# Kernel optimization log

Hardware: AMD Instinct MI355X
Metric: run time of the kernel (lower is better)

Reference implementation:

```python
import jax, jax.numpy as jnp
import numpy as np
import math

B, S, D, H = 8, 512, 1024, 16
HD = D // H  # 64
FF = 4 * D
EPS = 1e-5


def setup_inputs() -> dict:
    key = jax.random.key(0)
    ks = jax.random.split(key, 12)
    sc = 0.02
    return {
        "x":   jax.random.normal(ks[0], (B, S, D), jnp.float32),
        "Wq":  jax.random.normal(ks[1], (H, D, HD), jnp.float32) * sc,
        "Wk":  jax.random.normal(ks[2], (H, D, HD), jnp.float32) * sc,
        "Wv":  jax.random.normal(ks[3], (H, D, HD), jnp.float32) * sc,
        "Wo":  jax.random.normal(ks[4], (D, D), jnp.float32) * sc,
        "bo":  jnp.zeros((D,), jnp.float32),
        "g1":  jnp.ones((D,), jnp.float32),
        "b1":  jnp.zeros((D,), jnp.float32),
        "g2":  jnp.ones((D,), jnp.float32),
        "b2":  jnp.zeros((D,), jnp.float32),
        "W1":  jax.random.normal(ks[5], (D, FF), jnp.float32) * sc,
        "bf1": jnp.zeros((FF,), jnp.float32),
        "W2":  jax.random.normal(ks[6], (FF, D), jnp.float32) * sc,
        "bf2": jnp.zeros((D,), jnp.float32),
    }


def _layernorm(x, gamma, beta):
    # biased variance, matches torch.var(correction=0)
    mean = jnp.mean(x, axis=-1, keepdims=True)
    var = jnp.mean((x - mean) ** 2, axis=-1, keepdims=True)
    return (x - mean) / jnp.sqrt(var + EPS) * gamma + beta


def _block(x, Wq, Wk, Wv, Wo, bo, g1, b1, g2, b2, W1, bf1, W2, bf2):
    h = _layernorm(x, g1, b1)
    # per-head projections (no bias): [B,H,S,HD]
    Q = jnp.einsum("bsd,hde->bhse", h, Wq)
    K = jnp.einsum("bsd,hde->bhse", h, Wk)
    V = jnp.einsum("bsd,hde->bhse", h, Wv)
    scores = jnp.einsum("bhse,bhte->bhst", Q, K) / math.sqrt(HD)
    causal = jnp.triu(jnp.ones((S, S), bool), k=1)  # upper-triangular masked
    scores = jnp.where(causal, jnp.float32(-1e10), scores)
    att = jax.nn.softmax(scores, axis=-1)  # dropout in eval mode = identity
    ctx = jnp.einsum("bhst,bhte->bhse", att, V)
    # concat heads in order -> [B,S,D]
    ctx = ctx.transpose(0, 2, 1, 3).reshape(B, S, D)
    attn_out = ctx @ Wo + bo
    cache = attn_out + x
    h2 = _layernorm(cache, g2, b2)
    ff = jax.nn.gelu(h2 @ W1 + bf1, approximate=False) @ W2 + bf2
    return ff + cache


def reference(x, Wq, Wk, Wv, Wo, bo, g1, b1, g2, b2, W1, bf1, W2, bf2):
    return _block(x, Wq, Wk, Wv, Wo, bo, g1, b1, g2, b2, W1, bf1, W2, bf2)
```

## Files before the change

### kernel.cpp

```cpp
#include <hip/hip_runtime.h>
#include <hip/hip_bf16.h>

typedef __hip_bfloat16 bf16;

#define B_   8
#define S_   512
#define D_   1024
#define H_   16
#define HD_  64
#define FF_  4096
#define ROWS (B_ * S_)

typedef __attribute__((ext_vector_type(8))) unsigned short u16x8;
typedef __attribute__((ext_vector_type(4))) float f32x4;

typedef __attribute__((address_space(1))) const unsigned int GU32;
typedef __attribute__((address_space(3))) unsigned int LU32;
__device__ __forceinline__ void gld16(const void* g, void* l) {
    __builtin_amdgcn_global_load_lds((GU32*)g, (LU32*)l, 16, 0, 0);
}

__device__ __forceinline__ float bf2f(unsigned short u) {
    union { unsigned int i; float f; } v; v.i = ((unsigned int)u) << 16; return v.f;
}
__device__ __forceinline__ unsigned short f2bfu(float f) {
    bf16 h = __float2bfloat16(f);
    return *reinterpret_cast<unsigned short*>(&h);
}
__device__ __forceinline__ float ldsel(const void* p, size_t i, bool f32) {
    return f32 ? ((const float*)p)[i]
               : __bfloat162float(((const bf16*)p)[i]);
}
__device__ __forceinline__ float gelu_exact(float x) {
    return 0.5f * x * (1.f + erff(x * 0.70710678118654752440f));
}

__global__ __launch_bounds__(256) void ln_kernel(const void* __restrict__ x,
                                                 const void* __restrict__ gam,
                                                 const void* __restrict__ bet,
                                                 bf16* __restrict__ out,
                                                 int x_ws,
                                                 const unsigned short* __restrict__ probe) {
    bool pf32 = (probe[0] == 0);
    bool xf32 = (!x_ws) && pf32;
    int row = blockIdx.x;
    int tid = threadIdx.x;
    size_t rb = (size_t)row * D_;
    float v[4];
#pragma unroll
    for (int i = 0; i < 4; ++i) v[i] = ldsel(x, rb + tid + i * 256, xf32);
    float s  = v[0] + v[1] + v[2] + v[3];
    float s2 = v[0] * v[0] + v[1] * v[1] + v[2] * v[2] + v[3] * v[3];
#pragma unroll
    for (int off = 32; off > 0; off >>= 1) {
        s  += __shfl_down(s, off);
        s2 += __shfl_down(s2, off);
    }
    __shared__ float red[8];
    int wv = tid >> 6, ln = tid & 63;
    if (ln == 0) { red[wv] = s; red[4 + wv] = s2; }
    __syncthreads();
    s  = red[0] + red[1] + red[2] + red[3];
    s2 = red[4] + red[5] + red[6] + red[7];
    float mean = s * (1.f / 1024.f);
    float var  = s2 * (1.f / 1024.f) - mean * mean;
    float rstd = rsqrtf(var + 1e-5f);
#pragma unroll
    for (int i = 0; i < 4; ++i) {
        int c = tid + i * 256;
        float g = ldsel(gam, c, pf32), b = ldsel(bet, c, pf32);
        out[rb + c] = __float2bfloat16((v[i] - mean) * rstd * g + b);
    }
}

__global__ __launch_bounds__(256) void transpose_kernel(
    const void* __restrict__ src, bf16* __restrict__ dst,
    int N, int K, int sK, int sH,
    const unsigned short* __restrict__ probe) {
    bool pf32 = (probe[0] == 0);
    int tilesN = N >> 6;
    int tn = blockIdx.x % tilesN, tk = blockIdx.x / tilesN;
    int n0 = tn * 64, k0 = tk * 64;
    __shared__ float T[64][65];
    int t = threadIdx.x;
    size_t headoff = (size_t)(n0 >> 6) * sH;
#pragma unroll
    for (int i = 0; i < 16; ++i) {
        int lin = t + i * 256;
        int kl = lin >> 6, nl = lin & 63;
        size_t e = headoff + (size_t)(k0 + kl) * sK + nl;
        T[kl][nl] = ldsel(src, e, pf32);
    }
    __syncthreads();
#pragma unroll
    for (int i = 0; i < 16; ++i) {
        int lin = t + i * 256;
        int nl = lin >> 6, kl = lin & 63;
        dst[(size_t)(n0 + nl) * K + k0 + kl] = __float2bfloat16(T[kl][nl]);
    }
}

template<int BN>
__global__ __launch_bounds__(256) void gemm_mfma(
    const bf16* __restrict__ A, const bf16* __restrict__ Bt,
    int K, int nSeg, int segShift, size_t segStride,
    const void* __restrict__ bias,
    const void* __restrict__ resid, int resid_ws,
    bf16* __restrict__ outWS, void* __restrict__ outFinal, int mode,
    const unsigned short* __restrict__ probe) {
    constexpr int BM     = 128;
    constexpr int NR     = BN / 32;
    constexpr int PLANES = (BN == 64) ? 2 : 1;
    constexpr int KSTEP  = 32 * PLANES;
    constexpr int CPP    = 8 + BN / 16;
    constexpr int NCH    = PLANES * CPP / 4;
    constexpr int APL    = BM * 32;
    constexpr int BPL    = BN * 32;
    constexpr int AREG   = 2 * PLANES * APL;
    bool pf32 = (probe[0] == 0);
    __shared__ alignas(16) unsigned short SMEM[2 * PLANES * (BM + BN) * 32];
    int tid  = threadIdx.x;
    int lane = tid & 63, wv = tid >> 6;
    int g = lane >> 4, i16 = lane & 15;
    int wrow = wv >> 1, wcol = wv & 1;

    int GX = gridDim.x;
    int total = GX * gridDim.y;
    int bid = blockIdx.y * GX + blockIdx.x;
    int swz = bid;
    if ((total & 7) == 0) swz = (bid & 7) * (total >> 3) + (bid >> 3);
    int m0 = (swz / GX) * BM, n0 = (swz % GX) * BN;

    f32x4 acc[4][NR];
#pragma unroll
    for (int i = 0; i < 4; ++i)
#pragma unroll
        for (int j = 0; j < NR; ++j) acc[i][j] = (f32x4){0.f, 0.f, 0.f, 0.f};

    const unsigned short* gsrc[NCH];
    unsigned short* l0[NCH];
    unsigned short* l1[NCH];
    {
        int rl = lane >> 2, kq = (lane & 3) * 8;
#pragma unroll
        for (int c0 = 0; c0 < NCH; ++c0) {
            int c = c0 * 4 + wv;
            int pl = c / CPP, cc = c - pl * CPP;
            if (cc < 8) {
                gsrc[c0] = (const unsigned short*)A
                         + (size_t)(m0 + cc * 16 + rl) * K + pl * 32 + kq;
                l0[c0] = &SMEM[(0 * PLANES + pl) * APL + cc * 512];
                l1[c0] = &SMEM[(1 * PLANES + pl) * APL + cc * 512];
            } else {
                gsrc[c0] = (const unsigned short*)Bt
                         + (size_t)(n0 + (cc - 8) * 16 + rl) * K + pl * 32 + kq;
                l0[c0] = &SMEM[AREG + (0 * PLANES + pl) * BPL + (cc - 8) * 512];
                l1[c0] = &SMEM[AREG + (1 * PLANES + pl) * BPL + (cc - 8) * 512];
            }
        }
    }

#define STAGE0(KOFF) { _Pragma("unroll") \
    for (int c0 = 0; c0 < NCH; ++c0) gld16(gsrc[c0] + (KOFF), l0[c0]); }
#define STAGE1(KOFF) { _Pragma("unroll") \
    for (int c0 = 0; c0 < NCH; ++c0) gld16(gsrc[c0] + (KOFF), l1[c0]); }
#define COMPUTE(BUF) { \
    _Pragma("unroll") \
    for (int pl = 0; pl < PLANES; ++pl) { \
        u16x8 af[4], bfv[NR]; \
        _Pragma("unroll") \
        for (int i = 0; i < 4; ++i) \
            af[i] = *reinterpret_cast<const u16x8*>( \
                &SMEM[((BUF) * PLANES + pl) * APL + (wrow * 64 + i * 16 + i16) * 32 + g * 8]); \
        _Pragma("unroll") \
        for (int j = 0; j < NR; ++j) \
            bfv[j] = *reinterpret_cast<const u16x8*>( \
                &SMEM[AREG + ((BUF) * PLANES + pl) * BPL + (wcol * (BN / 2) + j * 16 + i16) * 32 + g * 8]); \
        _Pragma("unroll") \
        for (int i = 0; i < 4; ++i) \
            _Pragma("unroll") \
            for (int j = 0; j < NR; ++j) \
                asm("v_mfma_f32_16x16x32_bf16 %0, %1, %2, %0" \
                    : "+v"(acc[i][j]) : "v"(af[i]), "v"(bfv[j])); \
    } }

    STAGE0(0);
    __syncthreads();
    for (int k0 = 0; k0 < K; k0 += 2 * KSTEP) {
        STAGE1(k0 + KSTEP);
        COMPUTE(0);
        __syncthreads();
        if (k0 + 2 * KSTEP < K) STAGE0(k0 + 2 * KSTEP);
        COMPUTE(1);
        __syncthreads();
    }
#undef STAGE0
#undef STAGE1
#undef COMPUTE

    __builtin_amdgcn_sched_barrier(0);
    asm volatile("s_nop 7\n\ts_nop 7\n\ts_nop 7" ::: );
    __builtin_amdgcn_sched_barrier(0);

    if (outFinal && pf32) {
        int coll = i16, rowl = g * 4;
#pragma unroll
        for (int j = 0; j < NR; ++j) {
            int n = n0 + wcol * (BN / 2) + j * 16 + coll;
            int nl = n & (nSeg - 1);
            float bval = (mode != 0) ? ldsel(bias, nl, pf32) : 0.f;
#pragma unroll
            for (int i = 0; i < 4; ++i) {
                int mb = m0 + wrow * 64 + i * 16 + rowl;
#pragma unroll
                for (int r = 0; r < 4; ++r) {
                    size_t idx = (size_t)(mb + r) * nSeg + nl;
                    float c = acc[i][j][r];
                    if (mode == 1) {
                        c += bval;
                        c += resid_ws ? __bfloat162float(((const bf16*)resid)[idx])
                                      : ldsel(resid, idx, pf32);
                    } else if (mode == 2) {
                        c = gelu_exact(c + bval);
                    }
                    ((float*)outFinal)[idx] = c;
                }
            }
        }
    } else {
        unsigned short* Cs = SMEM;
        int seg = n0 >> segShift;
        int nl0 = n0 & (nSeg - 1);
        bf16* dst = outFinal ? (bf16*)outFinal
                             : outWS + (size_t)seg * segStride;
#pragma unroll
        for (int j = 0; j < NR; ++j) {
            int nloc = wcol * (BN / 2) + j * 16 + i16;
            int nl = nl0 + nloc;
            float bval = (mode != 0) ? ldsel(bias, nl, pf32) : 0.f;
#pragma unroll
            for (int i = 0; i < 4; ++i) {
#pragma unroll
                for (int r = 0; r < 4; ++r) {
                    int mloc = wrow * 64 + i * 16 + g * 4 + r;
                    float c = acc[i][j][r];
                    if (mode == 1) {
                        size_t idx = (size_t)(m0 + mloc) * nSeg + nl;
                        c += bval;
                        c += resid_ws ? __bfloat162float(((const bf16*)resid)[idx])
                                      : ldsel(resid, idx, pf32);
                    } else if (mode == 2) {
                        c = gelu_exact(c + bval);
                    }
                    int swzC = ((((mloc >> 2) & 3) ^ (mloc & 3)) << 4);
                    Cs[mloc * BN + (nloc ^ swzC)] = f2bfu(c);
                }
            }
        }
        __syncthreads();
        constexpr int NP = (BM * BN) / 2048;
#pragma unroll
        for (int p = 0; p < NP; ++p) {
            int lin = p * 2048 + tid * 8;
            int m = lin / BN, nn = lin % BN;
            int swzC = ((((m >> 2) & 3) ^ (m & 3)) << 4);
            u16x8 v = *reinterpret_cast<const u16x8*>(&Cs[m * BN + (nn ^ swzC)]);
            *reinterpret_cast<u16x8*>(dst + (size_t)(m0 + m) * nSeg + nl0 + nn) = v;
        }
    }
}

__global__ __launch_bounds__(256) void attn_kernel(const bf16* __restrict__ Qg,
                                                   const bf16* __restrict__ Kg,
                                                   const bf16* __restrict__ Vg,
                                                   bf16* __restrict__ Og) {
    constexpr int P = 72;
    __shared__ alignas(16) unsigned short Ks[64 * P];
    __shared__ alignas(16) unsigned short Vt[64 * P];
    __shared__ alignas(16) unsigned short Ps[64 * P];
    int qb = blockIdx.x;
    int bh = blockIdx.y;
    int b = bh >> 4, h = bh & 15;
    int tid = threadIdx.x;
    int lane = tid & 63, wv = tid >> 6;
    int g = lane >> 4, i16 = lane & 15;
    size_t base = ((size_t)b * S_) * D_ + h * HD_;

    u16x8 qa[2];
    {
        const unsigned short* qp = (const unsigned short*)Qg + base
            + (size_t)(qb * 64 + wv * 16 + i16) * D_ + g * 8;
#pragma unroll
        for (int kk = 0; kk < 2; ++kk) {
            u16x8 v = *reinterpret_cast<const u16x8*>(qp + kk * 32);
#pragma unroll
            for (int e = 0; e < 8; ++e) v[e] = f2bfu(bf2f(v[e]) * 0.125f);
            qa[kk] = v;
        }
    }
    f32x4 ov[4];
#pragma unroll
    for (int dj = 0; dj < 4; ++dj) ov[dj] = (f32x4){0.f, 0.f, 0.f, 0.f};
    float mrow[4], lrow[4];
#pragma unroll
    for (int r = 0; r < 4; ++r) { mrow[r] = -1e30f; lrow[r] = 0.f; }

    int st = tid >> 2, sd = (tid & 3) * 16;
    const unsigned short* Kp = (const unsigned short*)Kg + base + (size_t)st * D_ + sd;
    const unsigned short* Vp = (const unsigned short*)Vg + base + (size_t)st * D_ + sd;
    unsigned short* KsW = &Ks[st * P + sd];
    unsigned short* VtW = &Vt[sd * P + (st ^ sd)];
    int g1 = g >> 1, g0 = g & 1;
    unsigned short* PsW = &Ps[(wv * 16 + g * 4) * P + (i16 ^ (g0 << 3))];
    const unsigned short* PsR = &Ps[(wv * 16 + i16) * P + ((g ^ ((i16 >> 2) & 3)) << 3)];

    for (int kb = 0; kb <= qb; ++kb) {
        __syncthreads();
        size_t ko = (size_t)kb * 64 * D_;
        u16x8 k0 = *reinterpret_cast<const u16x8*>(Kp + ko);
        u16x8 k1 = *reinterpret_cast<const u16x8*>(Kp + ko + 8);
        u16x8 v0 = *reinterpret_cast<const u16x8*>(Vp + ko);
        u16x8 v1 = *reinterpret_cast<const u16x8*>(Vp + ko + 8);
        *reinterpret_cast<u16x8*>(KsW)     = k0;
        *reinterpret_cast<u16x8*>(KsW + 8) = k1;
#pragma unroll
        for (int ii = 0; ii < 8; ++ii) VtW[ii * P] = v0[ii];
#pragma unroll
        for (int ii = 0; ii < 8; ++ii) VtW[(ii + 8) * P] = v1[ii];
        __syncthreads();

        f32x4 sc[4];
#pragma unroll
        for (int tj = 0; tj < 4; ++tj) sc[tj] = (f32x4){0.f, 0.f, 0.f, 0.f};
#pragma unroll
        for (int kk = 0; kk < 2; ++kk)
#pragma unroll
            for (int tj = 0; tj < 4; ++tj) {
                u16x8 kf = *reinterpret_cast<const u16x8*>(
                    &Ks[(tj * 16 + i16) * P + kk * 32 + g * 8]);
                asm("v_mfma_f32_16x16x32_bf16 %0, %1, %2, %0"
                    : "+v"(sc[tj]) : "v"(qa[kk]), "v"(kf));
            }
        __builtin_amdgcn_sched_barrier(0);
        asm volatile("s_nop 7\n\ts_nop 7\n\ts_nop 7" ::: );
        __builtin_amdgcn_sched_barrier(0);

        if (kb == qb) {
#pragma unroll
            for (int tj = 0; tj < 4; ++tj)
#pragma unroll
                for (int r = 0; r < 4; ++r)
                    if (tj * 16 + i16 > wv * 16 + g * 4 + r) sc[tj][r] = -1e30f;
        }
        float al[4];
#pragma unroll
        for (int r = 0; r < 4; ++r) {
            float mt = fmaxf(fmaxf(sc[0][r], sc[1][r]), fmaxf(sc[2][r], sc[3][r]));
            mt = fmaxf(mt, __shfl_xor(mt, 1));
            mt = fmaxf(mt, __shfl_xor(mt, 2));
            mt = fmaxf(mt, __shfl_xor(mt, 4));
            mt = fmaxf(mt, __shfl_xor(mt, 8));
            float mnew = fmaxf(mrow[r], mt);
            al[r] = __expf(mrow[r] - mnew);
            mrow[r] = mnew;
        }
        float psum[4] = {0.f, 0.f, 0.f, 0.f};
        unsigned short pw[4][4];
#pragma unroll
        for (int tj = 0; tj < 4; ++tj)
#pragma unroll
            for (int r = 0; r < 4; ++r) {
                float p = __expf(sc[tj][r] - mrow[r]);
                unsigned short pb = f2bfu(p);
                pw[tj][r] = pb;
                psum[r] += bf2f(pb);
            }
#pragma unroll
        for (int r = 0; r < 4; ++r) {
            float ps = psum[r];
            ps += __shfl_xor(ps, 1);
            ps += __shfl_xor(ps, 2);
            ps += __shfl_xor(ps, 4);
            ps += __shfl_xor(ps, 8);
            lrow[r] = lrow[r] * al[r] + ps;
        }
#pragma unroll
        for (int dj = 0; dj < 4; ++dj)
#pragma unroll
            for (int r = 0; r < 4; ++r) ov[dj][r] *= al[r];
#pragma unroll
        for (int r = 0; r < 4; ++r)
#pragma unroll
            for (int tj = 0; tj < 4; ++tj)
                PsW[r * P + ((tj ^ g1) << 4)] = pw[tj][r];
#pragma unroll
        for (int kk = 0; kk < 2; ++kk) {
            u16x8 pf = *reinterpret_cast<const u16x8*>(PsR + kk * 32);
#pragma unroll
            for (int dj = 0; dj < 4; ++dj) {
                int tcol = ((kk << 5) | (g << 3)) ^ (dj << 4);
                u16x8 vf = *reinterpret_cast<const u16x8*>(
                    &Vt[(dj * 16 + i16) * P + tcol]);
                asm("v_mfma_f32_16x16x32_bf16 %0, %1, %2, %0"
                    : "+v"(ov[dj]) : "v"(pf), "v"(vf));
            }
        }
    }
    __builtin_amdgcn_sched_barrier(0);
    asm volatile("s_nop 7\n\ts_nop 7\n\ts_nop 7" ::: );
    __builtin_amdgcn_sched_barrier(0);
    float rl[4];
#pragma unroll
    for (int r = 0; r < 4; ++r) rl[r] = 1.f / lrow[r];
    bf16* op = Og + base + (size_t)(qb * 64 + wv * 16 + g * 4) * D_ + i16;
#pragma unroll
    for (int r = 0; r < 4; ++r)
#pragma unroll
        for (int dj = 0; dj < 4; ++dj)
            op[(size_t)r * D_ + dj * 16] = __float2bfloat16(ov[dj][r] * rl[r]);
}

extern "C" void kernel_launch(void* const* d_in, const int* in_sizes, int n_in,
                              void* d_out, int out_size, void* d_ws, size_t ws_size,
                              hipStream_t stream) {
    const void* x   = d_in[0];
    const void* Wq  = d_in[1];
    const void* Wk  = d_in[2];
    const void* Wv  = d_in[3];
    const void* Wo  = d_in[4];
    const void* bo  = d_in[5];
    const void* g1  = d_in[6];
    const void* b1  = d_in[7];
    const void* g2  = d_in[8];
    const void* b2  = d_in[9];
    const void* W1  = d_in[10];
    const void* bf1 = d_in[11];
    const void* W2  = d_in[12];
    const void* bf2 = d_in[13];
    const unsigned short* probe = (const unsigned short*)g1;

    bf16* ws = (bf16*)d_ws;
    const size_t Mi = (size_t)1024 * 1024;
    bf16* h     = ws;
    bf16* Qb    = ws + 4 * Mi;
    bf16* Kb    = ws + 8 * Mi;
    bf16* Vb    = ws + 12 * Mi;
    bf16* ctx   = ws;
    bf16* cache = ws + 4 * Mi;
    bf16* h2    = ws + 8 * Mi;
    bf16* ff1   = ws + 12 * Mi;
    bf16* WqT   = ws + 16 * Mi;
    bf16* WkT   = ws + 17 * Mi;
    bf16* WvT   = ws + 18 * Mi;
    bf16* WoT   = ws + 19 * Mi;
    bf16* W1T   = ws;
    bf16* W2T   = ws + 8 * Mi;

    transpose_kernel<<<256, 256, 0, stream>>>(Wq, WqT, 1024, 1024, HD_, D_ * HD_, probe);
    transpose_kernel<<<256, 256, 0, stream>>>(Wk, WkT, 1024, 1024, HD_, D_ * HD_, probe);
    transpose_kernel<<<256, 256, 0, stream>>>(Wv, WvT, 1024, 1024, HD_, D_ * HD_, probe);
    transpose_kernel<<<256, 256, 0, stream>>>(Wo, WoT, 1024, 1024, 1024, 64, probe);
    ln_kernel<<<ROWS, 256, 0, stream>>>(x, g1, b1, h, 0, probe);
    gemm_mfma<128><<<dim3(3072 / 128, ROWS / 128), 256, 0, stream>>>(
        h, WqT, 1024, 1024, 10, 4 * Mi,
        nullptr, nullptr, 0, Qb, nullptr, 0, probe);
    dim3 gA(S_ / 64, B_ * H_);
    attn_kernel<<<gA, 256, 0, stream>>>(Qb, Kb, Vb, ctx);
    gemm_mfma<64><<<dim3(1024 / 64, ROWS / 128), 256, 0, stream>>>(
        ctx, WoT, 1024, 1024, 30, 0,
        bo, x, 0, cache, nullptr, 1, probe);
    transpose_kernel<<<1024, 256, 0, stream>>>(W1, W1T, 4096, 1024, FF_, 64, probe);
    ln_kernel<<<ROWS, 256, 0, stream>>>(cache, g2, b2, h2, 1, probe);
    gemm_mfma<128><<<dim3(4096 / 128, ROWS / 128), 256, 0, stream>>>(
        h2, W1T, 1024, 4096, 30, 0,
        bf1, nullptr, 0, ff1, nullptr, 2, probe);
    transpose_kernel<<<1024, 256, 0, stream>>>(W2, W2T, 1024, 4096, 1024, 64, probe);
    gemm_mfma<64><<<dim3(1024 / 64, ROWS / 128), 256, 0, stream>>>(
        ff1, W2T, 4096, 1024, 30, 0,
        bf2, cache, 1, nullptr, d_out, 1, probe);
}
```

Before: 391.2 us.

## Triple-buffer the BN=128 GEMM main loop with counted vmcnt waits

For the BN=128 GEMM variant, the double-buffered LDS pipeline becomes a three-buffer ring. Async global-to-LDS loads are issued two K-steps ahead, and each step waits with `s_waitcnt vmcnt(4)` plus a raw barrier instead of a full `__syncthreads` drain. MFMA sections are wrapped in `s_setprio` to favour math waves, and a barrier is added before the epilogue reuses shared memory. The aim is to hide global load latency better, at the cost of 50% more LDS per block, which may reduce occupancy. The loop relies on K/32 being congruent to 2 mod 3.

```diff
diff --git a/kernel.cpp b/kernel.cpp
--- a/kernel.cpp
+++ b/kernel.cpp
@@ -111,14 +111,15 @@
     constexpr int BM     = 128;
     constexpr int NR     = BN / 32;
     constexpr int PLANES = (BN == 64) ? 2 : 1;
+    constexpr int NBUF   = (BN == 128) ? 3 : 2;
     constexpr int KSTEP  = 32 * PLANES;
     constexpr int CPP    = 8 + BN / 16;
     constexpr int NCH    = PLANES * CPP / 4;
     constexpr int APL    = BM * 32;
     constexpr int BPL    = BN * 32;
-    constexpr int AREG   = 2 * PLANES * APL;
+    constexpr int AREG   = NBUF * PLANES * APL;
     bool pf32 = (probe[0] == 0);
-    __shared__ alignas(16) unsigned short SMEM[2 * PLANES * (BM + BN) * 32];
+    __shared__ alignas(16) unsigned short SMEM[NBUF * PLANES * (BM + BN) * 32];
     int tid  = threadIdx.x;
     int lane = tid & 63, wv = tid >> 6;
     int g = lane >> 4, i16 = lane & 15;
@@ -138,8 +139,7 @@
         for (int j = 0; j < NR; ++j) acc[i][j] = (f32x4){0.f, 0.f, 0.f, 0.f};
 
     const unsigned short* gsrc[NCH];
-    unsigned short* l0[NCH];
-    unsigned short* l1[NCH];
+    unsigned short* ldst[NBUF][NCH];
     {
         int rl = lane >> 2, kq = (lane & 3) * 8;
 #pragma unroll
@@ -149,21 +149,24 @@
             if (cc < 8) {
                 gsrc[c0] = (const unsigned short*)A
                          + (size_t)(m0 + cc * 16 + rl) * K + pl * 32 + kq;
-                l0[c0] = &SMEM[(0 * PLANES + pl) * APL + cc * 512];
-                l1[c0] = &SMEM[(1 * PLANES + pl) * APL + cc * 512];
+#pragma unroll
+                for (int bb = 0; bb < NBUF; ++bb)
+                    ldst[bb][c0] = &SMEM[(bb * PLANES + pl) * APL + cc * 512];
             } else {
                 gsrc[c0] = (const unsigned short*)Bt
                          + (size_t)(n0 + (cc - 8) * 16 + rl) * K + pl * 32 + kq;
-                l0[c0] = &SMEM[AREG + (0 * PLANES + pl) * BPL + (cc - 8) * 512];
-                l1[c0] = &SMEM[AREG + (1 * PLANES + pl) * BPL + (cc - 8) * 512];
+#pragma unroll
+                for (int bb = 0; bb < NBUF; ++bb)
+                    ldst[bb][c0] = &SMEM[AREG + (bb * PLANES + pl) * BPL + (cc - 8) * 512];
             }
         }
     }
 
-#define STAGE0(KOFF) { _Pragma("unroll") \
-    for (int c0 = 0; c0 < NCH; ++c0) gld16(gsrc[c0] + (KOFF), l0[c0]); }
-#define STAGE1(KOFF) { _Pragma("unroll") \
-    for (int c0 = 0; c0 < NCH; ++c0) gld16(gsrc[c0] + (KOFF), l1[c0]); }
+#define STAGE(BUF, KOFF) { _Pragma("unroll") \
+    for (int c0 = 0; c0 < NCH; ++c0) gld16(gsrc[c0] + (KOFF), ldst[BUF][c0]); }
+#define WAITN  asm volatile("s_waitcnt vmcnt(4)" ::: "memory")
+#define WAIT0  asm volatile("s_waitcnt vmcnt(0)" ::: "memory")
+#define BARR { __builtin_amdgcn_s_barrier(); __builtin_amdgcn_sched_barrier(0); }
 #define COMPUTE(BUF) { \
     _Pragma("unroll") \
     for (int pl = 0; pl < PLANES; ++pl) { \
@@ -183,20 +186,40 @@
                 asm("v_mfma_f32_16x16x32_bf16 %0, %1, %2, %0" \
                     : "+v"(acc[i][j]) : "v"(af[i]), "v"(bfv[j])); \
     } }
-
-    STAGE0(0);
-    __syncthreads();
-    for (int k0 = 0; k0 < K; k0 += 2 * KSTEP) {
-        STAGE1(k0 + KSTEP);
-        COMPUTE(0);
+#define COMPUTE_P(BUF) { \
+    __builtin_amdgcn_s_setprio(1); \
+    COMPUTE(BUF) \
+    __builtin_amdgcn_s_setprio(0); }
+
+    if constexpr (BN == 64) {
+        STAGE(0, 0);
         __syncthreads();
-        if (k0 + 2 * KSTEP < K) STAGE0(k0 + 2 * KSTEP);
-        COMPUTE(1);
-        __syncthreads();
-    }
-#undef STAGE0
-#undef STAGE1
+        for (int k0 = 0; k0 < K; k0 += 2 * KSTEP) {
+            STAGE(1, k0 + KSTEP);
+            COMPUTE(0);
+            __syncthreads();
+            if (k0 + 2 * KSTEP < K) STAGE(0, k0 + 2 * KSTEP);
+            COMPUTE(1);
+            __syncthreads();
+        }
+    } else {
+        STAGE(0, 0); STAGE(1, 32);
+        int nsteps = K >> 5;
+        for (int t = 0; t + 5 <= nsteps; t += 3) {
+            int kb = t << 5;
+            WAITN; BARR; STAGE(2, kb + 64);  COMPUTE_P(0);
+            WAITN; BARR; STAGE(0, kb + 96);  COMPUTE_P(1);
+            WAITN; BARR; STAGE(1, kb + 128); COMPUTE_P(2);
+        }
+        WAITN; BARR; COMPUTE_P(0);
+        WAIT0; BARR; COMPUTE_P(1);
+    }
+#undef STAGE
+#undef WAITN
+#undef WAIT0
+#undef BARR
 #undef COMPUTE
+#undef COMPUTE_P
 
     __builtin_amdgcn_sched_barrier(0);
     asm volatile("s_nop 7\n\ts_nop 7\n\ts_nop 7" ::: );
@@ -228,6 +251,7 @@
             }
         }
     } else {
+        __syncthreads();
         unsigned short* Cs = SMEM;
         int seg = n0 >> segShift;
         int nl0 = n0 & (nSeg - 1);
```

New measurement: 398.9 us. No clear change (+2.0%).

## Merge QKV weight transposes into one launch and remap GEMM tile order per XCD

Applied to the files above, without the earlier changes.

The three Q/K/V weight transpose launches are merged into a single 768-block kernel that writes into contiguous WqT/WkT/WvT slots, removing two kernel launches. The GEMM block-to-tile mapping is also rewritten: each of the 8 dispatch slots (XCDs) now gets a 2x4 quadrant of the output grid, and tiles inside it are walked in groups of N columns. The aim is better L2 reuse of A and B tiles within each XCD. The new mapping only applies when the grid dimensions are divisible as required and otherwise falls back to the plain order.

```diff
diff --git a/kernel.cpp b/kernel.cpp
--- a/kernel.cpp
+++ b/kernel.cpp
@@ -73,13 +73,10 @@
     }
 }
 
-__global__ __launch_bounds__(256) void transpose_kernel(
-    const void* __restrict__ src, bf16* __restrict__ dst,
-    int N, int K, int sK, int sH,
-    const unsigned short* __restrict__ probe) {
-    bool pf32 = (probe[0] == 0);
+__device__ __forceinline__ void transpose_body(
+    const void* src, bf16* dst, int bid, int N, int K, int sK, int sH, bool pf32) {
     int tilesN = N >> 6;
-    int tn = blockIdx.x % tilesN, tk = blockIdx.x / tilesN;
+    int tn = bid % tilesN, tk = bid / tilesN;
     int n0 = tn * 64, k0 = tk * 64;
     __shared__ float T[64][65];
     int t = threadIdx.x;
@@ -98,6 +95,23 @@
         int nl = lin >> 6, kl = lin & 63;
         dst[(size_t)(n0 + nl) * K + k0 + kl] = __float2bfloat16(T[kl][nl]);
     }
+}
+
+__global__ __launch_bounds__(256) void transpose_kernel(
+    const void* __restrict__ src, bf16* __restrict__ dst,
+    int N, int K, int sK, int sH,
+    const unsigned short* __restrict__ probe) {
+    transpose_body(src, dst, blockIdx.x, N, K, sK, sH, probe[0] == 0);
+}
+
+__global__ __launch_bounds__(256) void transpose3_kernel(
+    const void* __restrict__ s0, const void* __restrict__ s1,
+    const void* __restrict__ s2, bf16* __restrict__ dst,
+    const unsigned short* __restrict__ probe) {
+    int which = blockIdx.x >> 8;
+    const void* src = (which == 0) ? s0 : ((which == 1) ? s1 : s2);
+    transpose_body(src, dst + (size_t)which * 1024 * 1024,
+                   blockIdx.x & 255, 1024, 1024, HD_, D_ * HD_, probe[0] == 0);
 }
 
 template<int BN>
@@ -124,12 +138,21 @@
     int g = lane >> 4, i16 = lane & 15;
     int wrow = wv >> 1, wcol = wv & 1;
 
-    int GX = gridDim.x;
-    int total = GX * gridDim.y;
+    int GX = gridDim.x, GY = gridDim.y;
+    int T = GX * GY;
     int bid = blockIdx.y * GX + blockIdx.x;
-    int swz = bid;
-    if ((total & 7) == 0) swz = (bid & 7) * (total >> 3) + (bid >> 3);
-    int m0 = (swz / GX) * BM, n0 = (swz % GX) * BN;
+    int bm, bn;
+    if (((T & 7) == 0) && ((GY & 3) == 0) && ((GX & 1) == 0)) {
+        int x = bid & 7, rank = bid >> 3;
+        int xr = x >> 1, xc = x & 1;
+        int MS = GY >> 2, NS = GX >> 1;
+        int G = (NS % 8 == 0) ? 8 : ((NS % 6 == 0) ? 6 : NS);
+        int ng = rank / (MS * G);
+        int rem = rank - ng * (MS * G);
+        int mloc = rem / G, nloc = ng * G + (rem - (rem / G) * G);
+        bm = xr * MS + mloc; bn = xc * NS + nloc;
+    } else { bm = blockIdx.y; bn = blockIdx.x; }
+    int m0 = bm * BM, n0 = bn * BN;
 
     f32x4 acc[4][NR];
 #pragma unroll
@@ -450,15 +473,11 @@
     bf16* h2    = ws + 8 * Mi;
     bf16* ff1   = ws + 12 * Mi;
     bf16* WqT   = ws + 16 * Mi;
-    bf16* WkT   = ws + 17 * Mi;
-    bf16* WvT   = ws + 18 * Mi;
     bf16* WoT   = ws + 19 * Mi;
     bf16* W1T   = ws;
     bf16* W2T   = ws + 8 * Mi;
 
-    transpose_kernel<<<256, 256, 0, stream>>>(Wq, WqT, 1024, 1024, HD_, D_ * HD_, probe);
-    transpose_kernel<<<256, 256, 0, stream>>>(Wk, WkT, 1024, 1024, HD_, D_ * HD_, probe);
-    transpose_kernel<<<256, 256, 0, stream>>>(Wv, WvT, 1024, 1024, HD_, D_ * HD_, probe);
+    transpose3_kernel<<<768, 256, 0, stream>>>(Wq, Wk, Wv, WqT, probe);
     transpose_kernel<<<256, 256, 0, stream>>>(Wo, WoT, 1024, 1024, 1024, 64, probe);
     ln_kernel<<<ROWS, 256, 0, stream>>>(x, g1, b1, h, 0, probe);
     gemm_mfma<128><<<dim3(3072 / 128, ROWS / 128), 256, 0, stream>>>(
```

New measurement: 381.1 us. 2.6% less time.
